# Kernel optimization log

Hardware: AMD Instinct MI355X
Metric: run time of the kernel (lower is better)

The kernel has to match this reference:

```python
import jax, jax.numpy as jnp
import numpy as np
import math

HIDDEN = 1024
HEADS = 8
HEAD = HIDDEN // HEADS
B, S = 2, 2048
SCALE_BASE = 512
EPS = 1e-5


def _xpos(x, downscale=False):
    # x: [..., S, d]  (canonical RetNet XPOS: rotate_every_two + xpos scaling)
    d = x.shape[-1]
    s = x.shape[-2]
    half = d // 2
    scale_vec = (jnp.arange(0, d, 2, dtype=jnp.float32) + 0.4 * d) / (1.4 * d)  # [half]
    pos = jnp.arange(s, dtype=jnp.float32)
    scale = scale_vec[None, :] ** (pos[:, None] / SCALE_BASE)                    # [S, half]
    inv_freq = 1.0 / (10000.0 ** (jnp.arange(half, dtype=jnp.float32) / half))
    ang = pos[:, None] * inv_freq[None, :]                                       # [S, half]
    sin, cos = jnp.sin(ang), jnp.cos(ang)
    if downscale:
        scale = 1.0 / scale
    sinp = jnp.repeat(sin * scale, 2, axis=-1)  # duplicate_interleave -> [S, d]
    cosp = jnp.repeat(cos * scale, 2, axis=-1)
    x1, x2 = x[..., ::2], x[..., 1::2]
    rot = jnp.stack([-x2, x1], axis=-1).reshape(x.shape)  # rotate_every_two
    return x * cosp + rot * sinp


def _gammas(h):
    return 1.0 - jnp.exp(jnp.linspace(math.log(1.0 / 32), math.log(1.0 / 512), h)).astype(jnp.float32)


def setup_inputs() -> dict:
    key = jax.random.key(0)
    ks = jax.random.split(key, 6)
    X = jax.random.normal(ks[0], (B, S, HIDDEN), dtype=jnp.float32)
    W_Q = jax.random.normal(ks[1], (HEADS, HIDDEN, HEAD), dtype=jnp.float32) / HIDDEN
    W_K = jax.random.normal(ks[2], (HEADS, HIDDEN, HEAD), dtype=jnp.float32) / HIDDEN
    W_V = jax.random.normal(ks[3], (HEADS, HIDDEN, HEAD), dtype=jnp.float32) / HIDDEN
    W_G = jax.random.normal(ks[4], (HIDDEN, HIDDEN), dtype=jnp.float32) / HIDDEN
    W_O = jax.random.normal(ks[5], (HIDDEN, HIDDEN), dtype=jnp.float32) / HIDDEN
    gn_weight = jnp.ones((HIDDEN,), dtype=jnp.float32)
    gn_bias = jnp.zeros((HIDDEN,), dtype=jnp.float32)
    return dict(X=X, W_Q=W_Q, W_K=W_K, W_V=W_V, W_G=W_G, W_O=W_O,
                gn_weight=gn_weight, gn_bias=gn_bias)


def reference(X, W_Q, W_K, W_V, W_G, W_O, gn_weight, gn_bias):
    b, s, _ = X.shape
    h, _, dv = W_V.shape
    Q = _xpos(jnp.einsum('bse,hed->bhsd', X, W_Q))
    K = _xpos(jnp.einsum('bse,hed->bhsd', X, W_K), downscale=True)
    V = jnp.einsum('bse,hed->bhsd', X, W_V)
    gam = _gammas(h)
    n = jnp.arange(s)
    diff = n[:, None] - n[None, :]
    mask = diff >= 0
    # per-head causal decay mask D[h, n, m] = gamma_h**(n-m) for n>=m else 0
    D = jnp.where(mask[None],
                  gam[:, None, None] ** jnp.where(mask, diff, 0)[None].astype(jnp.float32),
                  0.0)                                             # [H,S,S]
    scores = jnp.einsum('bhsd,bhtd->bhst', Q, K) * D[None]         # [B,H,S,S]
    Y = jnp.einsum('bhst,bhtv->bhsv', scores, V)                   # [B,H,S,dv]
    Y = jnp.transpose(Y, (0, 2, 1, 3))                             # [B,S,H,dv] (head concat)
    # GroupNorm(heads, v_dim) over flattened (B*S, v_dim): normalize within each head group
    mu = Y.mean(-1, keepdims=True)
    var = Y.var(-1, keepdims=True)
    Yn = ((Y - mu) / jnp.sqrt(var + EPS)).reshape(b, s, h * dv) * gn_weight + gn_bias
    gate = X @ W_G
    gate = gate * jax.nn.sigmoid(gate)  # swish
    return (gate * Yn) @ W_O
```

## Files before the change

kernel.cpp:

```cpp
#include <hip/hip_runtime.h>
#include <hip/hip_bf16.h>
#include <math.h>

namespace {

constexpr int Bc = 2;
constexpr int Sc = 2048;
constexpr int Ec = 1024;
constexpr int Hc = 8;
constexpr int Dc = 128;
constexpr int Mc = Bc * Sc;

typedef unsigned short u16;
typedef u16    u16x8  __attribute__((ext_vector_type(8)));
typedef u16    u16x4  __attribute__((ext_vector_type(4)));
typedef __bf16 bf16x8 __attribute__((ext_vector_type(8)));
typedef float  f32x4  __attribute__((ext_vector_type(4)));

static __device__ inline bf16x8 asbf(u16x8 v) { return __builtin_bit_cast(bf16x8, v); }

static __device__ inline f32x4 mfma16(u16x8 a, u16x8 b, f32x4 c) {
    return __builtin_amdgcn_mfma_f32_16x16x32_bf16(asbf(a), asbf(b), c, 0, 0, 0);
}

static __device__ inline u16 f2bf(float f) {
    unsigned u = __builtin_bit_cast(unsigned, f);
    return (u16)((u + 0x7fffu + ((u >> 16) & 1u)) >> 16);
}
static __device__ inline float bf2f(u16 h) {
    unsigned u = ((unsigned)h) << 16;
    return __builtin_bit_cast(float, u);
}

static __device__ inline void gload16(const u16* g, u16* l) {
    __builtin_amdgcn_global_load_lds(
        (__attribute__((address_space(1))) void*)const_cast<u16*>(g),
        (__attribute__((address_space(3))) void*)l,
        16, 0, 0);
}

#define AIDX(R_, hi_) (((R_) * 32) + (((hi_) ^ (((R_) >> 1) & 3)) << 3))

__global__ __launch_bounds__(256) void prep(const float* __restrict__ X,
                                            const float* __restrict__ W_Q,
                                            const float* __restrict__ W_K,
                                            const float* __restrict__ W_V,
                                            const float* __restrict__ W_G,
                                            const float* __restrict__ W_O,
                                            u16* __restrict__ Xb,
                                            u16* __restrict__ Wh,
                                            u16* __restrict__ Wsq,
                                            float2* __restrict__ tabQ,
                                            float2* __restrict__ tabK)
{
    const int bid = blockIdx.x, tid = threadIdx.x;
    __shared__ float tile[32][33];

    if (bid < 2048) {
        const int i = bid * 256 + tid;
        float4 a = *(const float4*)(X + (size_t)i * 8);
        float4 b = *(const float4*)(X + (size_t)i * 8 + 4);
        u16x8 o;
        o[0] = f2bf(a.x); o[1] = f2bf(a.y); o[2] = f2bf(a.z); o[3] = f2bf(a.w);
        o[4] = f2bf(b.x); o[5] = f2bf(b.y); o[6] = f2bf(b.z); o[7] = f2bf(b.w);
        *(u16x8*)(Xb + (size_t)i * 8) = o;
    } else if (bid < 5120) {
        const int idx = bid - 2048;
        const int z = idx >> 7, rem = idx & 127;
        const int r0 = (rem >> 2) * 32, c0 = (rem & 3) * 32;
        const float* ip = (z < 8 ? W_Q : z < 16 ? W_K : W_V) + (size_t)(z & 7) * Ec * Dc;
        u16* op = Wh + (size_t)z * Dc * Ec;
        const int ty = tid >> 5, tx = tid & 31;
#pragma unroll
        for (int i = ty; i < 32; i += 8) tile[i][tx] = ip[(size_t)(r0 + i) * Dc + c0 + tx];
        __syncthreads();
#pragma unroll
        for (int i = ty; i < 32; i += 8) op[(size_t)(c0 + i) * Ec + r0 + tx] = f2bf(tile[tx][i]);
    } else if (bid < 7168) {
        const int idx = bid - 5120;
        const int z = idx >> 10, rem = idx & 1023;
        const int r0 = (rem >> 5) * 32, c0 = (rem & 31) * 32;
        const float* ip = z == 0 ? W_G : W_O;
        u16* op = Wsq + (size_t)z * Ec * Ec;
        const int ty = tid >> 5, tx = tid & 31;
#pragma unroll
        for (int i = ty; i < 32; i += 8) tile[i][tx] = ip[(size_t)(r0 + i) * Ec + c0 + tx];
        __syncthreads();
#pragma unroll
        for (int i = ty; i < 32; i += 8) op[(size_t)(c0 + i) * Ec + r0 + tx] = f2bf(tile[tx][i]);
    } else {
        const int i = (bid - 7168) * 256 + tid;
        const int s = i >> 6, ip = i & 63;
        float sv = (2.f * (float)ip + 51.2f) * (1.f / 179.2f);
        float sc = exp2f(((float)s * (1.f / 512.f)) * log2f(sv));
        float freq = exp2f(-(float)ip * (13.287712379549449f / 64.f));
        float ang = (float)s * freq;
        float sn, cs;
        sincosf(ang, &sn, &cs);
        tabQ[i] = make_float2(cs * sc, sn * sc);
        tabK[i] = make_float2(cs / sc, sn / sc);
    }
}

__global__ __launch_bounds__(512, 2) void mgemm4(const u16* __restrict__ A,
                                                 const u16* __restrict__ Ball,
                                                 u16* __restrict__ Qo,
                                                 u16* __restrict__ Ko,
                                                 u16* __restrict__ Vo,
                                                 u16* __restrict__ Go,
                                                 const float2* __restrict__ tabQ,
                                                 const float2* __restrict__ tabK)
{
    const int t = threadIdx.x, lane = t & 63, wid = t >> 6;
    const int wm = wid >> 2, wn = wid & 3;
    const int rl = lane & 15, hi = lane >> 4;
    const int r0 = blockIdx.x * 256;
    const int wsel = blockIdx.y >> 2;
    const int n0 = (blockIdx.y & 3) * 256;
    const u16* Bt = Ball + (size_t)wsel * Ec * Ec;

    __shared__ u16 lds[2][2][256 * 64];

    f32x4 acc[8][4] = {};

    const int srow = lane >> 3;
    const int scol = (((lane & 7) ^ srow) << 3);
    const u16* Asrc = A  + (size_t)(r0 + wid * 32 + srow) * Ec + scol;
    const u16* Bsrc = Bt + (size_t)(n0 + wid * 32 + srow) * Ec + scol;

#define STAGE256(tile, buf)                                                     \
    do {                                                                        \
        const int _k0 = (tile) * 64;                                            \
        _Pragma("unroll")                                                       \
        for (int i = 0; i < 4; ++i) {                                           \
            gload16(Asrc + (size_t)(i * 8) * Ec + _k0,                          \
                    &lds[buf][0][(wid * 32 + i * 8) * 64]);                     \
            gload16(Bsrc + (size_t)(i * 8) * Ec + _k0,                          \
                    &lds[buf][1][(wid * 32 + i * 8) * 64]);                     \
        }                                                                       \
    } while (0)

    STAGE256(0, 0);
    for (int tt = 0; tt < 16; ++tt) {
        const int buf = tt & 1;
        if (tt + 1 < 16) {
            STAGE256(tt + 1, buf ^ 1);
            asm volatile("s_waitcnt vmcnt(8)" ::: "memory");
        } else {
            asm volatile("s_waitcnt vmcnt(0)" ::: "memory");
        }
        __builtin_amdgcn_s_barrier();

        u16x8 breg[4][2];
#pragma unroll
        for (int cf = 0; cf < 4; ++cf)
#pragma unroll
            for (int ks = 0; ks < 2; ++ks) {
                const int row = wn * 64 + cf * 16 + rl;
                breg[cf][ks] = *(const u16x8*)
                    &lds[buf][1][row * 64 + ((ks * 32 + hi * 8) ^ ((rl & 7) << 3))];
            }
#pragma unroll
        for (int q = 0; q < 4; ++q) {
            u16x8 areg[2][2];
#pragma unroll
            for (int rfi = 0; rfi < 2; ++rfi)
#pragma unroll
                for (int ks = 0; ks < 2; ++ks) {
                    const int row = wm * 128 + (q * 2 + rfi) * 16 + rl;
                    areg[rfi][ks] = *(const u16x8*)
                        &lds[buf][0][row * 64 + ((ks * 32 + hi * 8) ^ ((rl & 7) << 3))];
                }
            __builtin_amdgcn_s_setprio(1);
#pragma unroll
            for (int rfi = 0; rfi < 2; ++rfi)
#pragma unroll
                for (int cf = 0; cf < 4; ++cf)
#pragma unroll
                    for (int ks = 0; ks < 2; ++ks)
                        acc[q * 2 + rfi][cf] =
                            mfma16(breg[cf][ks], areg[rfi][ks], acc[q * 2 + rfi][cf]);
            __builtin_amdgcn_s_setprio(0);
        }
        __builtin_amdgcn_s_barrier();
    }
#undef STAGE256

    u16* Cout = wsel == 0 ? Qo : wsel == 1 ? Ko : wsel == 2 ? Vo : Go;
    const float2* tab = wsel == 0 ? tabQ : tabK;

#pragma unroll
    for (int rf = 0; rf < 8; ++rf) {
        const int row = r0 + wm * 128 + rf * 16 + rl;
#pragma unroll
        for (int cf = 0; cf < 4; ++cf) {
            const int col0 = n0 + wn * 64 + cf * 16 + hi * 4;
            f32x4 v = acc[rf][cf];
            if (wsel <= 1) {
                const size_t tb = (size_t)(row & 2047) * 64 + ((col0 >> 1) & 63);
                const float2 c0 = tab[tb];
                const float2 c1 = tab[tb + 1];
                float e0 = v[0], o0 = v[1], e1 = v[2], o1 = v[3];
                v[0] = e0 * c0.x - o0 * c0.y;
                v[1] = o0 * c0.x + e0 * c0.y;
                v[2] = e1 * c1.x - o1 * c1.y;
                v[3] = o1 * c1.x + e1 * c1.y;
            } else if (wsel == 3) {
#pragma unroll
                for (int r = 0; r < 4; ++r) v[r] = v[r] / (1.f + expf(-v[r]));
            }
            u16x4 pk;
#pragma unroll
            for (int r = 0; r < 4; ++r) pk[r] = f2bf(v[r]);
            *(u16x4*)(Cout + (size_t)row * Ec + col0) = pk;
        }
    }
}

__global__ __launch_bounds__(256) void mgemmO(const u16* __restrict__ A,
                                              const u16* __restrict__ Bt,
                                              float* __restrict__ Cout)
{
    const int t = threadIdx.x, lane = t & 63, w = t >> 6;
    const int rl = lane & 15, hi = lane >> 4;
    const int r0 = blockIdx.x * 128;
    const int n0 = blockIdx.y * 64;

    __shared__ u16 Ab[2][128 * 32];
    __shared__ u16 Bb[2][64 * 32];

    f32x4 acc[2][4] = {};

    const int srow = lane >> 2;
    const int schunk = (lane & 3) ^ ((lane >> 3) & 3);
    const u16* Asrc = A  + (size_t)(r0 + w * 32 + srow) * Ec + schunk * 8;
    const u16* Bsrc = Bt + (size_t)(n0 + w * 16 + srow) * Ec + schunk * 8;

#define STAGEO(tile_, buf_)                                                   \
    do {                                                                      \
        const int _k0 = (tile_) * 32;                                         \
        gload16(Asrc + _k0,                   &Ab[buf_][(w * 32) * 32]);      \
        gload16(Asrc + (size_t)16 * Ec + _k0, &Ab[buf_][(w * 32 + 16) * 32]); \
        gload16(Bsrc + _k0,                   &Bb[buf_][(w * 16) * 32]);      \
    } while (0)

    STAGEO(0, 0);
    for (int tt = 0; tt < 32; ++tt) {
        const int buf = tt & 1;
        if (tt + 1 < 32) {
            STAGEO(tt + 1, buf ^ 1);
            asm volatile("s_waitcnt vmcnt(3)" ::: "memory");
        } else {
            asm volatile("s_waitcnt vmcnt(0)" ::: "memory");
        }
        __builtin_amdgcn_s_barrier();

        u16x8 breg[4], areg[2];
#pragma unroll
        for (int cf = 0; cf < 4; ++cf)
            breg[cf] = *(const u16x8*)&Bb[buf][AIDX(cf * 16 + rl, hi)];
#pragma unroll
        for (int rfi = 0; rfi < 2; ++rfi)
            areg[rfi] = *(const u16x8*)&Ab[buf][AIDX(w * 32 + rfi * 16 + rl, hi)];
        __builtin_amdgcn_s_setprio(1);
#pragma unroll
        for (int rfi = 0; rfi < 2; ++rfi)
#pragma unroll
            for (int cf = 0; cf < 4; ++cf)
                acc[rfi][cf] = mfma16(breg[cf], areg[rfi], acc[rfi][cf]);
        __builtin_amdgcn_s_setprio(0);
        __builtin_amdgcn_s_barrier();
    }
#undef STAGEO

#pragma unroll
    for (int rfi = 0; rfi < 2; ++rfi) {
        const int row = r0 + w * 32 + rfi * 16 + rl;
#pragma unroll
        for (int cf = 0; cf < 4; ++cf) {
            const int col0 = n0 + cf * 16 + hi * 4;
            *(f32x4*)(Cout + (size_t)row * Ec + col0) = acc[rfi][cf];
        }
    }
}

__global__ __launch_bounds__(256) void ret_gn(const u16* __restrict__ Q,
                                              const u16* __restrict__ K,
                                              const u16* __restrict__ V,
                                              const u16* __restrict__ G,
                                              const float* __restrict__ gw,
                                              const float* __restrict__ gbias,
                                              u16* __restrict__ Z)
{
    const int t = threadIdx.x, lane = t & 63, w = t >> 6;
    const int rl = lane & 15, hi = lane >> 4;
    const int id = blockIdx.x;
    const int slot = id & 15;
    const int a  = id >> 4;
    const int rb = (a < 16) ? (31 - a) : (a - 16);
    const int b = slot >> 3;
    const int h = b == 0 ? (slot & 7) : 7 - (slot & 7);

    __shared__ u16 Ks[64][136];
    __shared__ u16 Vt[128][68];
    __shared__ u16 Ss[64][72];

    const float lga = -3.4657359027997265f;
    const float lgb = -6.2383246250395075f;
    const float gamma = 1.f - expf(lga + (float)h * (lgb - lga) * (1.f / 7.f));
    const float lg2 = log2f(gamma);

    int c_lo = 0;
    {
        float cut = 9.2103404f / (-logf(gamma));
        int mmin = rb * 64 - (int)cut;
        if (mmin > 0) c_lo = mmin >> 6;
    }

    const int ki = t >> 2,        kq = (t & 3) * 32;
    const int vm4 = (t & 15) * 4, vd = (t >> 4) * 8;
    const u16* Kg0 = K + (size_t)(b * Sc) * Ec + h * Dc;
    const u16* Vg0 = V + (size_t)(b * Sc) * Ec + h * Dc;

    u16x8 kreg[4], vreg[4];
    {
        const u16* Kg = Kg0 + (size_t)(c_lo * 64 + ki) * Ec + kq;
#pragma unroll
        for (int r = 0; r < 4; ++r) kreg[r] = *(const u16x8*)(Kg + r * 8);
        const u16* Vg = Vg0 + (size_t)(c_lo * 64 + vm4) * Ec + vd;
#pragma unroll
        for (int r = 0; r < 4; ++r) vreg[r] = *(const u16x8*)(Vg + (size_t)r * Ec);
    }

    {
        const int i = t >> 2, q = (t & 3) * 32;
        const u16* Qg = Q + (size_t)(b * Sc + rb * 64 + i) * Ec + h * Dc + q;
        u16x8 v0 = *(const u16x8*)(Qg);
        u16x8 v1 = *(const u16x8*)(Qg + 8);
        u16x8 v2 = *(const u16x8*)(Qg + 16);
        u16x8 v3 = *(const u16x8*)(Qg + 24);
        *(u16x8*)&Ks[i][q]      = v0;
        *(u16x8*)&Ks[i][q + 8]  = v1;
        *(u16x8*)&Ks[i][q + 16] = v2;
        *(u16x8*)&Ks[i][q + 24] = v3;
    }
    __syncthreads();
    u16x8 qf[4][4];
#pragma unroll
    for (int nt = 0; nt < 4; ++nt)
#pragma unroll
        for (int ks = 0; ks < 4; ++ks)
            qf[nt][ks] = *(const u16x8*)&Ks[nt * 16 + rl][ks * 32 + hi * 8];
    __syncthreads();

    float mf[4];
#pragma unroll
    for (int reg = 0; reg < 4; ++reg)
        mf[reg] = exp2f(-lg2 * (float)(w * 16 + hi * 4 + reg));
    float nf[4];
#pragma unroll
    for (int nt = 0; nt < 4; ++nt)
        nf[nt] = exp2f(lg2 * (float)((rb - c_lo) * 64 + nt * 16 + rl));
    const float ginv64 = exp2f(-lg2 * 64.f);

    f32x4 yacc[8] = {};

    for (int c = c_lo; c <= rb; ++c) {
#pragma unroll
        for (int r = 0; r < 4; ++r)
            *(u16x8*)&Ks[ki][kq + r * 8] = kreg[r];
#pragma unroll
        for (int j = 0; j < 8; ++j) {
            u16x4 p;
            p[0] = vreg[0][j]; p[1] = vreg[1][j]; p[2] = vreg[2][j]; p[3] = vreg[3][j];
            *(u16x4*)&Vt[vd + j][vm4] = p;
        }
        __syncthreads();
        if (c < rb) {
            const u16* Kg = Kg0 + (size_t)((c + 1) * 64 + ki) * Ec + kq;
#pragma unroll
            for (int r = 0; r < 4; ++r) kreg[r] = *(const u16x8*)(Kg + r * 8);
            const u16* Vg = Vg0 + (size_t)((c + 1) * 64 + vm4) * Ec + vd;
#pragma unroll
            for (int r = 0; r < 4; ++r) vreg[r] = *(const u16x8*)(Vg + (size_t)r * Ec);
        }

        __builtin_amdgcn_s_setprio(1);
        u16x8 kf[4];
#pragma unroll
        for (int ks = 0; ks < 4; ++ks)
            kf[ks] = *(const u16x8*)&Ks[w * 16 + rl][ks * 32 + hi * 8];
#pragma unroll
        for (int nt = 0; nt < 4; ++nt) {
            f32x4 s = {};
#pragma unroll
            for (int ks = 0; ks < 4; ++ks)
                s = mfma16(kf[ks], qf[nt][ks], s);
            u16x4 pk;
#pragma unroll
            for (int reg = 0; reg < 4; ++reg) {
                float wgt = nf[nt] * mf[reg];
                if (c == rb && (w * 16 + hi * 4 + reg) > (nt * 16 + rl)) wgt = 0.f;
                pk[reg] = f2bf(s[reg] * wgt);
            }
            *(u16x4*)&Ss[nt * 16 + rl][w * 16 + hi * 4] = pk;
        }
        __builtin_amdgcn_s_setprio(0);
        __syncthreads();

        u16x8 sf0 = *(const u16x8*)&Ss[w * 16 + rl][hi * 8];
        u16x8 sf1 = *(const u16x8*)&Ss[w * 16 + rl][32 + hi * 8];
        __builtin_amdgcn_s_setprio(1);
#pragma unroll
        for (int ct = 0; ct < 8; ++ct) {
            u16x8 vf0 = *(const u16x8*)&Vt[ct * 16 + rl][hi * 8];
            u16x8 vf1 = *(const u16x8*)&Vt[ct * 16 + rl][32 + hi * 8];
            yacc[ct] = mfma16(vf0, sf0, yacc[ct]);
            yacc[ct] = mfma16(vf1, sf1, yacc[ct]);
        }
        __builtin_amdgcn_s_setprio(0);
        __syncthreads();
#pragma unroll
        for (int nt = 0; nt < 4; ++nt) nf[nt] *= ginv64;
    }

    const int nloc = w * 16 + rl;
    const size_t row = (size_t)(b * Sc + rb * 64 + nloc);
    float s = 0.f, sq = 0.f;
#pragma unroll
    for (int ct = 0; ct < 8; ++ct)
#pragma unroll
        for (int reg = 0; reg < 4; ++reg) {
            float v = yacc[ct][reg];
            s += v; sq += v * v;
        }
    s  += __shfl_xor(s, 16);  sq += __shfl_xor(sq, 16);
    s  += __shfl_xor(s, 32);  sq += __shfl_xor(sq, 32);
    const float mu  = s * (1.f / 128.f);
    const float var = sq * (1.f / 128.f) - mu * mu;
    const float inv = rsqrtf(var + 1e-5f);
#pragma unroll
    for (int ct = 0; ct < 8; ++ct) {
        const int col0 = h * Dc + ct * 16 + hi * 4;
        const f32x4 w4 = *(const f32x4*)(gw + col0);
        const f32x4 b4 = *(const f32x4*)(gbias + col0);
        const u16x4 g4 = *(const u16x4*)(G + row * Ec + col0);
        u16x4 z4;
#pragma unroll
        for (int reg = 0; reg < 4; ++reg)
            z4[reg] = f2bf(((yacc[ct][reg] - mu) * inv * w4[reg] + b4[reg]) * bf2f(g4[reg]));
        *(u16x4*)(Z + row * Ec + col0) = z4;
    }
}

}

extern "C" void kernel_launch(void* const* d_in, const int* in_sizes, int n_in,
                              void* d_out, int out_size, void* d_ws, size_t ws_size,
                              hipStream_t stream)
{
    const float* X    = (const float*)d_in[0];
    const float* W_Q  = (const float*)d_in[1];
    const float* W_K  = (const float*)d_in[2];
    const float* W_V  = (const float*)d_in[3];
    const float* W_G  = (const float*)d_in[4];
    const float* W_O  = (const float*)d_in[5];
    const float* gw   = (const float*)d_in[6];
    const float* gb   = (const float*)d_in[7];

    char* ws = (char*)d_ws;
    const size_t NX = (size_t)Mc * Ec;
    u16*    Xb   = (u16*)ws;                ws += NX * 2;
    u16*    WqT  = (u16*)ws;                ws += (size_t)Ec * Ec * 2;
    u16*    WkT  = (u16*)ws;                ws += (size_t)Ec * Ec * 2;
    u16*    WvT  = (u16*)ws;                ws += (size_t)Ec * Ec * 2;
    u16*    WgT  = (u16*)ws;                ws += (size_t)Ec * Ec * 2;
    u16*    WoT  = (u16*)ws;                ws += (size_t)Ec * Ec * 2;
    float2* tabQ = (float2*)ws;             ws += (size_t)Sc * 64 * sizeof(float2);
    float2* tabK = (float2*)ws;             ws += (size_t)Sc * 64 * sizeof(float2);
    u16*    Qb   = (u16*)ws;                ws += NX * 2;
    u16*    Kb   = (u16*)ws;                ws += NX * 2;
    u16*    Vb   = (u16*)ws;                ws += NX * 2;
    u16*    Gb   = (u16*)ws;                ws += NX * 2;
    u16*    Zb   = (u16*)ws;                ws += NX * 2;
    (void)WkT; (void)WvT;

    prep<<<dim3(7680), dim3(256), 0, stream>>>(X, W_Q, W_K, W_V, W_G, W_O,
                                               Xb, WqT, WgT, tabQ, tabK);

    mgemm4<<<dim3(Mc / 256, 16), dim3(512), 0, stream>>>(Xb, WqT, Qb, Kb, Vb, Gb, tabQ, tabK);

    ret_gn<<<dim3(512), dim3(256), 0, stream>>>(Qb, Kb, Vb, Gb, gw, gb, Zb);

    mgemmO<<<dim3(Mc / 128, Ec / 64), dim3(256), 0, stream>>>(Zb, WoT, (float*)d_out);
}
```

Before: 126.2 us.

## Process 128 query rows per block in retention kernel to share K/V tiles

The retention+groupnorm kernel now uses 512-thread blocks covering 128 query rows (two groups of four waves) instead of 64. Each K/V chunk loaded to shared memory is reused by both query groups, which halves global K/V traffic and staging work per output row. The cost is half as many blocks (256 on a large GPU) and some wasted MFMA work on masked-out chunks for the lower group. The reversed block ordering that balanced causal work across blocks is also dropped.

```diff
diff --git a/kernel.cpp b/kernel.cpp
--- a/kernel.cpp
+++ b/kernel.cpp
@@ -12,6 +12,7 @@
 constexpr int Mc = Bc * Sc;
 
 typedef unsigned short u16;
+typedef unsigned int   u32;
 typedef u16    u16x8  __attribute__((ext_vector_type(8)));
 typedef u16    u16x4  __attribute__((ext_vector_type(4)));
 typedef __bf16 bf16x8 __attribute__((ext_vector_type(8)));
@@ -284,7 +285,7 @@
     }
 }
 
-__global__ __launch_bounds__(256) void ret_gn(const u16* __restrict__ Q,
+__global__ __launch_bounds__(512) void ret_gn(const u16* __restrict__ Q,
                                               const u16* __restrict__ K,
                                               const u16* __restrict__ V,
                                               const u16* __restrict__ G,
@@ -292,18 +293,18 @@
                                               const float* __restrict__ gbias,
                                               u16* __restrict__ Z)
 {
-    const int t = threadIdx.x, lane = t & 63, w = t >> 6;
+    const int t = threadIdx.x, lane = t & 63, wid = t >> 6;
+    const int w4 = wid & 3, g = wid >> 2;
     const int rl = lane & 15, hi = lane >> 4;
     const int id = blockIdx.x;
     const int slot = id & 15;
-    const int a  = id >> 4;
-    const int rb = (a < 16) ? (31 - a) : (a - 16);
+    const int rb = id >> 4;
     const int b = slot >> 3;
     const int h = b == 0 ? (slot & 7) : 7 - (slot & 7);
 
     __shared__ u16 Ks[64][136];
     __shared__ u16 Vt[128][68];
-    __shared__ u16 Ss[64][72];
+    __shared__ u16 Ss[128][72];
 
     const float lga = -3.4657359027997265f;
     const float lgb = -6.2383246250395075f;
@@ -313,83 +314,80 @@
     int c_lo = 0;
     {
         float cut = 9.2103404f / (-logf(gamma));
-        int mmin = rb * 64 - (int)cut;
+        int mmin = rb * 128 - (int)cut;
         if (mmin > 0) c_lo = mmin >> 6;
     }
-
-    const int ki = t >> 2,        kq = (t & 3) * 32;
-    const int vm4 = (t & 15) * 4, vd = (t >> 4) * 8;
+    const int c_hi = 2 * rb + 1;
+
+    const int ki = t >> 3,        kq = (t & 7) * 16;
+    const int vm2 = (t & 31) * 2, vd = (t >> 5) * 8;
     const u16* Kg0 = K + (size_t)(b * Sc) * Ec + h * Dc;
     const u16* Vg0 = V + (size_t)(b * Sc) * Ec + h * Dc;
 
-    u16x8 kreg[4], vreg[4];
+    u16x8 kreg[2], vreg[2];
     {
         const u16* Kg = Kg0 + (size_t)(c_lo * 64 + ki) * Ec + kq;
-#pragma unroll
-        for (int r = 0; r < 4; ++r) kreg[r] = *(const u16x8*)(Kg + r * 8);
-        const u16* Vg = Vg0 + (size_t)(c_lo * 64 + vm4) * Ec + vd;
-#pragma unroll
-        for (int r = 0; r < 4; ++r) vreg[r] = *(const u16x8*)(Vg + (size_t)r * Ec);
-    }
-
-    {
-        const int i = t >> 2, q = (t & 3) * 32;
-        const u16* Qg = Q + (size_t)(b * Sc + rb * 64 + i) * Ec + h * Dc + q;
-        u16x8 v0 = *(const u16x8*)(Qg);
-        u16x8 v1 = *(const u16x8*)(Qg + 8);
-        u16x8 v2 = *(const u16x8*)(Qg + 16);
-        u16x8 v3 = *(const u16x8*)(Qg + 24);
-        *(u16x8*)&Ks[i][q]      = v0;
-        *(u16x8*)&Ks[i][q + 8]  = v1;
-        *(u16x8*)&Ks[i][q + 16] = v2;
-        *(u16x8*)&Ks[i][q + 24] = v3;
+        kreg[0] = *(const u16x8*)(Kg);
+        kreg[1] = *(const u16x8*)(Kg + 8);
+        const u16* Vg = Vg0 + (size_t)(c_lo * 64 + vm2) * Ec + vd;
+        vreg[0] = *(const u16x8*)(Vg);
+        vreg[1] = *(const u16x8*)(Vg + Ec);
+    }
+
+    u16x8 qf[4][4];
+#pragma unroll
+    for (int pass = 0; pass < 2; ++pass) {
+        const u16* Qg = Q + (size_t)(b * Sc + rb * 128 + pass * 64 + ki) * Ec + h * Dc + kq;
+        u16x8 q0 = *(const u16x8*)(Qg);
+        u16x8 q1 = *(const u16x8*)(Qg + 8);
+        __syncthreads();
+        *(u16x8*)&Ks[ki][kq]     = q0;
+        *(u16x8*)&Ks[ki][kq + 8] = q1;
+        __syncthreads();
+        if (g == pass) {
+#pragma unroll
+            for (int nt = 0; nt < 4; ++nt)
+#pragma unroll
+                for (int ks = 0; ks < 4; ++ks)
+                    qf[nt][ks] = *(const u16x8*)&Ks[nt * 16 + rl][ks * 32 + hi * 8];
+        }
     }
     __syncthreads();
-    u16x8 qf[4][4];
+
+    float mf[4];
+#pragma unroll
+    for (int reg = 0; reg < 4; ++reg)
+        mf[reg] = exp2f(-lg2 * (float)(w4 * 16 + hi * 4 + reg));
+    float nf[4];
 #pragma unroll
     for (int nt = 0; nt < 4; ++nt)
-#pragma unroll
-        for (int ks = 0; ks < 4; ++ks)
-            qf[nt][ks] = *(const u16x8*)&Ks[nt * 16 + rl][ks * 32 + hi * 8];
-    __syncthreads();
-
-    float mf[4];
-#pragma unroll
-    for (int reg = 0; reg < 4; ++reg)
-        mf[reg] = exp2f(-lg2 * (float)(w * 16 + hi * 4 + reg));
-    float nf[4];
-#pragma unroll
-    for (int nt = 0; nt < 4; ++nt)
-        nf[nt] = exp2f(lg2 * (float)((rb - c_lo) * 64 + nt * 16 + rl));
+        nf[nt] = exp2f(lg2 * (float)(rb * 128 + g * 64 + nt * 16 + rl - c_lo * 64));
     const float ginv64 = exp2f(-lg2 * 64.f);
 
     f32x4 yacc[8] = {};
 
-    for (int c = c_lo; c <= rb; ++c) {
-#pragma unroll
-        for (int r = 0; r < 4; ++r)
-            *(u16x8*)&Ks[ki][kq + r * 8] = kreg[r];
-#pragma unroll
-        for (int j = 0; j < 8; ++j) {
-            u16x4 p;
-            p[0] = vreg[0][j]; p[1] = vreg[1][j]; p[2] = vreg[2][j]; p[3] = vreg[3][j];
-            *(u16x4*)&Vt[vd + j][vm4] = p;
-        }
-        __syncthreads();
-        if (c < rb) {
+    for (int c = c_lo; c <= c_hi; ++c) {
+        *(u16x8*)&Ks[ki][kq]     = kreg[0];
+        *(u16x8*)&Ks[ki][kq + 8] = kreg[1];
+#pragma unroll
+        for (int j = 0; j < 8; ++j)
+            *(u32*)&Vt[vd + j][vm2] = (u32)vreg[0][j] | ((u32)vreg[1][j] << 16);
+        __syncthreads();
+        if (c < c_hi) {
             const u16* Kg = Kg0 + (size_t)((c + 1) * 64 + ki) * Ec + kq;
-#pragma unroll
-            for (int r = 0; r < 4; ++r) kreg[r] = *(const u16x8*)(Kg + r * 8);
-            const u16* Vg = Vg0 + (size_t)((c + 1) * 64 + vm4) * Ec + vd;
-#pragma unroll
-            for (int r = 0; r < 4; ++r) vreg[r] = *(const u16x8*)(Vg + (size_t)r * Ec);
+            kreg[0] = *(const u16x8*)(Kg);
+            kreg[1] = *(const u16x8*)(Kg + 8);
+            const u16* Vg = Vg0 + (size_t)((c + 1) * 64 + vm2) * Ec + vd;
+            vreg[0] = *(const u16x8*)(Vg);
+            vreg[1] = *(const u16x8*)(Vg + Ec);
         }
 
         __builtin_amdgcn_s_setprio(1);
         u16x8 kf[4];
 #pragma unroll
         for (int ks = 0; ks < 4; ++ks)
-            kf[ks] = *(const u16x8*)&Ks[w * 16 + rl][ks * 32 + hi * 8];
+            kf[ks] = *(const u16x8*)&Ks[w4 * 16 + rl][ks * 32 + hi * 8];
+        const int cg = 2 * rb + g;
 #pragma unroll
         for (int nt = 0; nt < 4; ++nt) {
             f32x4 s = {};
@@ -400,16 +398,17 @@
 #pragma unroll
             for (int reg = 0; reg < 4; ++reg) {
                 float wgt = nf[nt] * mf[reg];
-                if (c == rb && (w * 16 + hi * 4 + reg) > (nt * 16 + rl)) wgt = 0.f;
+                if (c > cg || (c == cg && (w4 * 16 + hi * 4 + reg) > (nt * 16 + rl)))
+                    wgt = 0.f;
                 pk[reg] = f2bf(s[reg] * wgt);
             }
-            *(u16x4*)&Ss[nt * 16 + rl][w * 16 + hi * 4] = pk;
+            *(u16x4*)&Ss[g * 64 + nt * 16 + rl][w4 * 16 + hi * 4] = pk;
         }
         __builtin_amdgcn_s_setprio(0);
         __syncthreads();
 
-        u16x8 sf0 = *(const u16x8*)&Ss[w * 16 + rl][hi * 8];
-        u16x8 sf1 = *(const u16x8*)&Ss[w * 16 + rl][32 + hi * 8];
+        u16x8 sf0 = *(const u16x8*)&Ss[wid * 16 + rl][hi * 8];
+        u16x8 sf1 = *(const u16x8*)&Ss[wid * 16 + rl][32 + hi * 8];
         __builtin_amdgcn_s_setprio(1);
 #pragma unroll
         for (int ct = 0; ct < 8; ++ct) {
@@ -424,8 +423,8 @@
         for (int nt = 0; nt < 4; ++nt) nf[nt] *= ginv64;
     }
 
-    const int nloc = w * 16 + rl;
-    const size_t row = (size_t)(b * Sc + rb * 64 + nloc);
+    const int nloc = wid * 16 + rl;
+    const size_t row = (size_t)(b * Sc + rb * 128 + nloc);
     float s = 0.f, sq = 0.f;
 #pragma unroll
     for (int ct = 0; ct < 8; ++ct)
@@ -442,13 +441,13 @@
 #pragma unroll
     for (int ct = 0; ct < 8; ++ct) {
         const int col0 = h * Dc + ct * 16 + hi * 4;
-        const f32x4 w4 = *(const f32x4*)(gw + col0);
+        const f32x4 w4v = *(const f32x4*)(gw + col0);
         const f32x4 b4 = *(const f32x4*)(gbias + col0);
         const u16x4 g4 = *(const u16x4*)(G + row * Ec + col0);
         u16x4 z4;
 #pragma unroll
         for (int reg = 0; reg < 4; ++reg)
-            z4[reg] = f2bf(((yacc[ct][reg] - mu) * inv * w4[reg] + b4[reg]) * bf2f(g4[reg]));
+            z4[reg] = f2bf(((yacc[ct][reg] - mu) * inv * w4v[reg] + b4[reg]) * bf2f(g4[reg]));
         *(u16x4*)(Z + row * Ec + col0) = z4;
     }
 }
@@ -490,7 +489,7 @@
 
     mgemm4<<<dim3(Mc / 256, 16), dim3(512), 0, stream>>>(Xb, WqT, Qb, Kb, Vb, Gb, tabQ, tabK);
 
-    ret_gn<<<dim3(512), dim3(256), 0, stream>>>(Qb, Kb, Vb, Gb, gw, gb, Zb);
+    ret_gn<<<dim3(256), dim3(512), 0, stream>>>(Qb, Kb, Vb, Gb, gw, gb, Zb);
 
     mgemmO<<<dim3(Mc / 128, Ec / 64), dim3(256), 0, stream>>>(Zb, WoT, (float*)d_out);
 }
```

Result: slower. 138.3 us (+9.6%).
